# Optimization experiments

Hardware: AMD Instinct MI355X
Metric: run time of the kernel (lower is better)

The kernel has to match this reference:

```python
import jax, jax.numpy as jnp
import numpy as np

N_NODES = 100000


def _gcn_norm(edge_index, n):
    # Add self loops and compute symmetric normalization deg^-1/2 A_hat deg^-1/2
    loops = jnp.arange(n, dtype=edge_index.dtype)
    row = jnp.concatenate([edge_index[0], loops])  # source nodes [E+N]
    col = jnp.concatenate([edge_index[1], loops])  # target nodes [E+N]
    ones = jnp.ones(row.shape[0], dtype=jnp.float32)
    deg = jax.ops.segment_sum(ones, col, num_segments=n)  # in-degree incl. self loop
    dinv = jnp.where(deg > 0, jax.lax.rsqrt(deg), 0.0)
    norm = dinv[row] * dinv[col]  # [E+N]
    return row, col, norm


def _gcn_conv(x, W, b, row, col, norm, n):
    h = x @ W                     # [N, out]
    msg = h[row] * norm[:, None]  # gather + scale  [E+N, out]
    agg = jax.ops.segment_sum(msg, col, num_segments=n)  # scatter-add
    return agg + b


def setup_inputs() -> dict:
    key = jax.random.key(0)
    ks = jax.random.split(key, 8)
    n, e, din, dh, dout = N_NODES, 1600000, 128, 128, 64
    x = jax.random.normal(ks[0], (n, din), dtype=jnp.float32)
    edge_index = jax.random.randint(ks[1], (2, e), 0, n, dtype=jnp.int64)
    s = lambda fan: 1.0 / np.sqrt(fan)
    W0 = jax.random.normal(ks[2], (din, dh), dtype=jnp.float32) * s(din)
    W1 = jax.random.normal(ks[3], (dh, dh), dtype=jnp.float32) * s(dh)
    W2 = jax.random.normal(ks[4], (dh, dout), dtype=jnp.float32) * s(dh)
    b0 = jnp.zeros((dh,), jnp.float32)
    b1 = jnp.zeros((dh,), jnp.float32)
    b2 = jnp.zeros((dout,), jnp.float32)
    return {"x": x, "edge_index": edge_index, "W0": W0, "b0": b0,
            "W1": W1, "b1": b1, "W2": W2, "b2": b2}


def reference(x, edge_index, W0, b0, W1, b1, W2, b2):
    # Eval-mode forward (dropout inactive), matching GCN.forward
    n = x.shape[0]
    row, col, norm = _gcn_norm(edge_index, n)
    h = jax.nn.relu(_gcn_conv(x, W0, b0, row, col, norm, n))
    h = jax.nn.relu(_gcn_conv(h, W1, b1, row, col, norm, n))
    out = _gcn_conv(h, W2, b2, row, col, norm, n)
    return out
```

## Files before the change

### kernel.cpp

```cpp
#include <hip/hip_runtime.h>
#include <stdint.h>


static inline size_t ws_align(size_t x) { return (x + 255) & ~(size_t)255; }

typedef float __f2 __attribute__((ext_vector_type(2)));
typedef float __f4 __attribute__((ext_vector_type(4)));

__device__ __forceinline__ int eidx(const void* p, size_t i, int is64) {
  return is64 ? (int)((const long long*)p)[i] : ((const int*)p)[i];
}

__device__ __forceinline__ uint16_t f2bf(float f) {
  uint32_t u = __float_as_uint(f);
  u += 0x7fffu + ((u >> 16) & 1u);
  return (uint16_t)(u >> 16);
}
__device__ __forceinline__ float bf_lo(uint32_t h) { return __uint_as_float(h << 16); }
__device__ __forceinline__ float bf_hi(uint32_t h) { return __uint_as_float(h & 0xffff0000u); }

__global__ void detect_k(const int* ei, int* flag) {
  if (threadIdx.x == 0 && blockIdx.x == 0) {
    int allz = 1;
    for (int i = 1; i < 128; i += 2)
      if (ei[i] != 0) { allz = 0; break; }
    *flag = allz;
  }
}

__global__ __launch_bounds__(256) void passA_k(const void* ei, const int* __restrict__ flag,
                                               int* __restrict__ bucket_cnt, int E, int NB) {
  __shared__ int cnt[256];
  int t = threadIdx.x;
  cnt[t] = 0;
  __syncthreads();
  int is64 = *flag;
  for (int e = blockIdx.x * 256 + t; e < E; e += gridDim.x * 256) {
    int c = eidx(ei, (size_t)E + e, is64);
    atomicAdd(&cnt[c >> 9], 1);
  }
  __syncthreads();
  if (t < NB && cnt[t]) atomicAdd(&bucket_cnt[t], cnt[t]);
}

__global__ __launch_bounds__(256) void bscan_k(const int* __restrict__ bucket_cnt,
                                               int* __restrict__ bucket_offs,
                                               int* __restrict__ gcursor, int NB) {
  __shared__ int sh[256];
  int t = threadIdx.x;
  int v = (t < NB) ? bucket_cnt[t] : 0;
  sh[t] = v;
  __syncthreads();
  for (int off = 1; off < 256; off <<= 1) {
    int x = (t >= off) ? sh[t - off] : 0;
    __syncthreads();
    sh[t] += x;
    __syncthreads();
  }
  if (t < NB) {
    int excl = sh[t] - v;
    bucket_offs[t] = excl;
    gcursor[t] = excl;
  }
  if (t == NB - 1) bucket_offs[NB] = sh[t];
}

__global__ __launch_bounds__(256) void passB_k(const void* ei, const int* __restrict__ flag,
                                               int* __restrict__ gcursor,
                                               int2* __restrict__ epk_binned, int E, int NB) {
  __shared__ int2 sorted[4096];
  __shared__ int cnt[256], bbase[256], gb[256], cur[256];
  const int t = threadIdx.x;
  const int base = blockIdx.x * 4096;
  const int CH = min(4096, E - base);
  const int is64 = *flag;

  cnt[t] = 0;
  __syncthreads();
  for (int i = t; i < CH; i += 256) {
    int c = eidx(ei, (size_t)E + base + i, is64);
    atomicAdd(&cnt[c >> 9], 1);
  }
  __syncthreads();
  {
    int v = cnt[t];
    __shared__ int sh[256];
    sh[t] = v;
    __syncthreads();
    for (int off = 1; off < 256; off <<= 1) {
      int x = (t >= off) ? sh[t - off] : 0;
      __syncthreads();
      sh[t] += x;
      __syncthreads();
    }
    bbase[t] = sh[t] - v;
    gb[t] = (t < NB && v) ? atomicAdd(&gcursor[t], v) : 0;
    cur[t] = 0;
  }
  __syncthreads();
  for (int i = t; i < CH; i += 256) {
    int r = eidx(ei, (size_t)base + i, is64);
    int c = eidx(ei, (size_t)E + base + i, is64);
    int b = c >> 9;
    int rank = atomicAdd(&cur[b], 1);
    sorted[bbase[b] + rank] = make_int2(r, c);
  }
  __syncthreads();
  for (int i = t; i < CH; i += 256) {
    int2 v = sorted[i];
    int b = v.y >> 9;
    epk_binned[gb[b] + (i - bbase[b])] = v;
  }
}

__global__ __launch_bounds__(256) void passC0_k(const int2* __restrict__ epk_binned,
                                                const int* __restrict__ bucket_offs,
                                                int* __restrict__ deg, int* __restrict__ offs,
                                                int n, int NB) {
  __shared__ int dcnt[512];
  __shared__ int s[256];
  const int t = threadIdx.x;
  const int b = blockIdx.x;
  dcnt[t] = 0; dcnt[t + 256] = 0;
  __syncthreads();
  const int lo = bucket_offs[b], hi = bucket_offs[b + 1];
  for (int i = lo + t; i < hi; i += 256)
    atomicAdd(&dcnt[epk_binned[i].y & 511], 1);
  __syncthreads();
  int d0 = dcnt[2 * t], d1 = dcnt[2 * t + 1];
  int pv = d0 + d1;
  s[t] = pv;
  __syncthreads();
  for (int off = 1; off < 256; off <<= 1) {
    int x = (t >= off) ? s[t - off] : 0;
    __syncthreads();
    s[t] += x;
    __syncthreads();
  }
  int pex = s[t] - pv;
  const int node0 = b << 9;
  int g0 = node0 + 2 * t, g1 = node0 + 2 * t + 1;
  if (g0 < n) { deg[g0] = d0; offs[g0] = lo + pex; }
  if (g1 < n) { deg[g1] = d1; offs[g1] = lo + pex + d0; }
  if (b == NB - 1 && t == 0) offs[n] = hi;
}

__global__ void dinv_k(const int* __restrict__ deg, float* __restrict__ dinv, int n) {
  int i = blockIdx.x * blockDim.x + threadIdx.x;
  if (i < n) dinv[i] = rsqrtf((float)deg[i] + 1.0f);
}

__global__ __launch_bounds__(256) void passC_k(const int2* __restrict__ epk_binned,
                                               const int* __restrict__ bucket_offs,
                                               const int* __restrict__ offs,
                                               uint32_t* __restrict__ epk) {
  __shared__ int cur[512];
  const int t = threadIdx.x;
  const int b = blockIdx.x;
  cur[t] = 0; cur[t + 256] = 0;
  __syncthreads();
  const int lo = bucket_offs[b], hi = bucket_offs[b + 1];
  for (int i = lo + t; i < hi; i += 256) {
    int2 v = epk_binned[i];
    int pos = offs[v.y] + atomicAdd(&cur[v.y & 511], 1);
    epk[pos] = (uint32_t)v.x;
  }
}

template <int COLS, bool SLICED_IN>
__global__ __launch_bounds__(256) void gemm_k(const float* __restrict__ X,
                                              const float* __restrict__ W,
                                              const float* __restrict__ dinv,
                                              uint16_t* __restrict__ H, int N) {
  constexpr int KB = 32;
  constexpr int CG = COLS / 8;
  constexpr int RG = 256 / CG;
  constexpr int ROWS = RG * 8;
  constexpr int XP = ROWS + 4;

  __shared__ float Xs[KB][XP];
  __shared__ float Ws[KB][COLS];

  const int tid = threadIdx.x;
  const int cg = tid % CG, rg = tid / CG;
  const int c0 = cg * 8, rr0 = rg * 8;
  const int rowbase = blockIdx.x * ROWS;
  const float4* X4 = (const float4*)X;

  float acc[8][8];
#pragma unroll
  for (int a = 0; a < 8; ++a)
#pragma unroll
    for (int b = 0; b < 8; ++b) acc[a][b] = 0.f;

  for (int k0 = 0; k0 < 128; k0 += KB) {
    __syncthreads();
#pragma unroll
    for (int i = tid; i < KB * (COLS / 4); i += 256) {
      int kk = i / (COLS / 4);
      int cc = i % (COLS / 4);
      float4 w = ((const float4*)(W + (size_t)(k0 + kk) * COLS))[cc];
      ((float4*)&Ws[kk][0])[cc] = w;
    }
#pragma unroll
    for (int i = tid; i < ROWS * (KB / 4); i += 256) {
      int rr = i / (KB / 4);
      int k4 = i % (KB / 4);
      int gr = rowbase + rr;
      if (gr >= N) gr = N - 1;
      float4 xv;
      if (SLICED_IN) {
        int k = k0 + k4 * 4;
        int s = k >> 5, q = (k & 31) >> 2;
        xv = X4[((size_t)s * N + gr) * 8 + q];
      } else {
        xv = X4[(size_t)gr * 32 + (k0 >> 2) + k4];
      }
      Xs[k4 * 4 + 0][rr] = xv.x;
      Xs[k4 * 4 + 1][rr] = xv.y;
      Xs[k4 * 4 + 2][rr] = xv.z;
      Xs[k4 * 4 + 3][rr] = xv.w;
    }
    __syncthreads();
#pragma unroll 2
    for (int k = 0; k < KB; ++k) {
      float4 xa = *(const float4*)&Xs[k][rr0];
      float4 xb = *(const float4*)&Xs[k][rr0 + 4];
      float4 wa = *(const float4*)&Ws[k][c0];
      float4 wb = *(const float4*)&Ws[k][c0 + 4];
      float xr[8] = {xa.x, xa.y, xa.z, xa.w, xb.x, xb.y, xb.z, xb.w};
      float wr[8] = {wa.x, wa.y, wa.z, wa.w, wb.x, wb.y, wb.z, wb.w};
#pragma unroll
      for (int a = 0; a < 8; ++a)
#pragma unroll
        for (int b = 0; b < 8; ++b) acc[a][b] = fmaf(xr[a], wr[b], acc[a][b]);
    }
  }
  uint32_t* HW = (uint32_t*)H;
  const int wbase = c0 >> 1;
  const int sl = wbase >> 4;
  const int woff = wbase & 15;
#pragma unroll
  for (int a = 0; a < 8; ++a) {
    int row = rowbase + rr0 + a;
    if (row < N) {
      float sc = dinv[row];
      uint32_t p[4];
#pragma unroll
      for (int q = 0; q < 4; ++q)
        p[q] = (uint32_t)f2bf(sc * acc[a][2 * q]) | ((uint32_t)f2bf(sc * acc[a][2 * q + 1]) << 16);
      uint4 ov = make_uint4(p[0], p[1], p[2], p[3]);
      *(uint4*)&HW[((size_t)sl * N + row) * 16 + woff] = ov;
    }
  }
}

__global__ __launch_bounds__(256, 8) void agg128s_k(const uint32_t* __restrict__ HW,
                                                    const int* __restrict__ offs,
                                                    const uint32_t* __restrict__ epk,
                                                    const float* __restrict__ bias,
                                                    float* __restrict__ Aout,
                                                    int relu, int N) {
  const int s = blockIdx.x & 3;
  const int g = blockIdx.x >> 2;
  const int lane = threadIdx.x & 63;
  const int wid = threadIdx.x >> 6;
  const int d = lane >> 3, w = lane & 7;
  const int c = g * 32 + wid * 8 + d;
  if (c >= N) return;
  const uint32_t* Hs = HW + (size_t)s * N * 16;
  int e0 = offs[c], e1 = offs[c + 1];
  float a0 = 0.f, a1 = 0.f, a2 = 0.f, a3 = 0.f;
  int e = e0;
  for (; e + 8 <= e1; e += 8) {
    uint32_t p0 = epk[e],     p1 = epk[e + 1], p2 = epk[e + 2], p3 = epk[e + 3];
    uint32_t p4 = epk[e + 4], p5 = epk[e + 5], p6 = epk[e + 6], p7 = epk[e + 7];
    uint2 h0 = *(const uint2*)&Hs[(size_t)p0 * 16 + 2 * w];
    uint2 h1 = *(const uint2*)&Hs[(size_t)p1 * 16 + 2 * w];
    uint2 h2 = *(const uint2*)&Hs[(size_t)p2 * 16 + 2 * w];
    uint2 h3 = *(const uint2*)&Hs[(size_t)p3 * 16 + 2 * w];
    uint2 h4 = *(const uint2*)&Hs[(size_t)p4 * 16 + 2 * w];
    uint2 h5 = *(const uint2*)&Hs[(size_t)p5 * 16 + 2 * w];
    uint2 h6 = *(const uint2*)&Hs[(size_t)p6 * 16 + 2 * w];
    uint2 h7 = *(const uint2*)&Hs[(size_t)p7 * 16 + 2 * w];
    a0 += bf_lo(h0.x); a1 += bf_hi(h0.x); a2 += bf_lo(h0.y); a3 += bf_hi(h0.y);
    a0 += bf_lo(h1.x); a1 += bf_hi(h1.x); a2 += bf_lo(h1.y); a3 += bf_hi(h1.y);
    a0 += bf_lo(h2.x); a1 += bf_hi(h2.x); a2 += bf_lo(h2.y); a3 += bf_hi(h2.y);
    a0 += bf_lo(h3.x); a1 += bf_hi(h3.x); a2 += bf_lo(h3.y); a3 += bf_hi(h3.y);
    a0 += bf_lo(h4.x); a1 += bf_hi(h4.x); a2 += bf_lo(h4.y); a3 += bf_hi(h4.y);
    a0 += bf_lo(h5.x); a1 += bf_hi(h5.x); a2 += bf_lo(h5.y); a3 += bf_hi(h5.y);
    a0 += bf_lo(h6.x); a1 += bf_hi(h6.x); a2 += bf_lo(h6.y); a3 += bf_hi(h6.y);
    a0 += bf_lo(h7.x); a1 += bf_hi(h7.x); a2 += bf_lo(h7.y); a3 += bf_hi(h7.y);
  }
  for (; e + 4 <= e1; e += 4) {
    uint32_t p0 = epk[e], p1 = epk[e + 1], p2 = epk[e + 2], p3 = epk[e + 3];
    uint2 h0 = *(const uint2*)&Hs[(size_t)p0 * 16 + 2 * w];
    uint2 h1 = *(const uint2*)&Hs[(size_t)p1 * 16 + 2 * w];
    uint2 h2 = *(const uint2*)&Hs[(size_t)p2 * 16 + 2 * w];
    uint2 h3 = *(const uint2*)&Hs[(size_t)p3 * 16 + 2 * w];
    a0 += bf_lo(h0.x); a1 += bf_hi(h0.x); a2 += bf_lo(h0.y); a3 += bf_hi(h0.y);
    a0 += bf_lo(h1.x); a1 += bf_hi(h1.x); a2 += bf_lo(h1.y); a3 += bf_hi(h1.y);
    a0 += bf_lo(h2.x); a1 += bf_hi(h2.x); a2 += bf_lo(h2.y); a3 += bf_hi(h2.y);
    a0 += bf_lo(h3.x); a1 += bf_hi(h3.x); a2 += bf_lo(h3.y); a3 += bf_hi(h3.y);
  }
  for (; e < e1; ++e) {
    uint2 h = *(const uint2*)&Hs[(size_t)epk[e] * 16 + 2 * w];
    a0 += bf_lo(h.x); a1 += bf_hi(h.x); a2 += bf_lo(h.y); a3 += bf_hi(h.y);
  }
  float dc = rsqrtf((float)(e1 - e0) + 1.f);
  uint2 hc = *(const uint2*)&Hs[(size_t)c * 16 + 2 * w];
  float r0 = fmaf(dc, a0 + bf_lo(hc.x), bias[s * 32 + 4 * w + 0]);
  float r1 = fmaf(dc, a1 + bf_hi(hc.x), bias[s * 32 + 4 * w + 1]);
  float r2 = fmaf(dc, a2 + bf_lo(hc.y), bias[s * 32 + 4 * w + 2]);
  float r3 = fmaf(dc, a3 + bf_hi(hc.y), bias[s * 32 + 4 * w + 3]);
  if (relu) {
    r0 = fmaxf(r0, 0.f); r1 = fmaxf(r1, 0.f);
    r2 = fmaxf(r2, 0.f); r3 = fmaxf(r3, 0.f);
  }
  __f4 res; res.x = r0; res.y = r1; res.z = r2; res.w = r3;
  __builtin_nontemporal_store(res, (__f4*)(Aout + ((size_t)s * N + c) * 32 + 4 * w));
}

__global__ __launch_bounds__(256, 8) void agg64s_k(const uint32_t* __restrict__ HW,
                                                   const int* __restrict__ offs,
                                                   const uint32_t* __restrict__ epk,
                                                   const float* __restrict__ bias,
                                                   float* __restrict__ out, int N) {
  const int r = blockIdx.x & 7;
  const int s = r >> 2;
  const int quar = r & 3;
  const int ng = (N + 31) >> 5;
  const int nq = (ng + 3) >> 2;
  const int g = quar * nq + (blockIdx.x >> 3);
  if (g >= ng) return;
  const int lane = threadIdx.x & 63;
  const int wid = threadIdx.x >> 6;
  const int d = lane >> 3, w = lane & 7;
  const int c = g * 32 + wid * 8 + d;
  if (c >= N) return;
  const uint32_t* Hs = HW + (size_t)s * N * 16;
  int e0 = offs[c], e1 = offs[c + 1];
  float a0 = 0.f, a1 = 0.f, a2 = 0.f, a3 = 0.f;
  int e = e0;
  for (; e + 8 <= e1; e += 8) {
    uint32_t p0 = epk[e],     p1 = epk[e + 1], p2 = epk[e + 2], p3 = epk[e + 3];
    uint32_t p4 = epk[e + 4], p5 = epk[e + 5], p6 = epk[e + 6], p7 = epk[e + 7];
    uint2 h0 = *(const uint2*)&Hs[(size_t)p0 * 16 + 2 * w];
    uint2 h1 = *(const uint2*)&Hs[(size_t)p1 * 16 + 2 * w];
    uint2 h2 = *(const uint2*)&Hs[(size_t)p2 * 16 + 2 * w];
    uint2 h3 = *(const uint2*)&Hs[(size_t)p3 * 16 + 2 * w];
    uint2 h4 = *(const uint2*)&Hs[(size_t)p4 * 16 + 2 * w];
    uint2 h5 = *(const uint2*)&Hs[(size_t)p5 * 16 + 2 * w];
    uint2 h6 = *(const uint2*)&Hs[(size_t)p6 * 16 + 2 * w];
    uint2 h7 = *(const uint2*)&Hs[(size_t)p7 * 16 + 2 * w];
    a0 += bf_lo(h0.x); a1 += bf_hi(h0.x); a2 += bf_lo(h0.y); a3 += bf_hi(h0.y);
    a0 += bf_lo(h1.x); a1 += bf_hi(h1.x); a2 += bf_lo(h1.y); a3 += bf_hi(h1.y);
    a0 += bf_lo(h2.x); a1 += bf_hi(h2.x); a2 += bf_lo(h2.y); a3 += bf_hi(h2.y);
    a0 += bf_lo(h3.x); a1 += bf_hi(h3.x); a2 += bf_lo(h3.y); a3 += bf_hi(h3.y);
    a0 += bf_lo(h4.x); a1 += bf_hi(h4.x); a2 += bf_lo(h4.y); a3 += bf_hi(h4.y);
    a0 += bf_lo(h5.x); a1 += bf_hi(h5.x); a2 += bf_lo(h5.y); a3 += bf_hi(h5.y);
    a0 += bf_lo(h6.x); a1 += bf_hi(h6.x); a2 += bf_lo(h6.y); a3 += bf_hi(h6.y);
    a0 += bf_lo(h7.x); a1 += bf_hi(h7.x); a2 += bf_lo(h7.y); a3 += bf_hi(h7.y);
  }
  for (; e + 4 <= e1; e += 4) {
    uint32_t p0 = epk[e], p1 = epk[e + 1], p2 = epk[e + 2], p3 = epk[e + 3];
    uint2 h0 = *(const uint2*)&Hs[(size_t)p0 * 16 + 2 * w];
    uint2 h1 = *(const uint2*)&Hs[(size_t)p1 * 16 + 2 * w];
    uint2 h2 = *(const uint2*)&Hs[(size_t)p2 * 16 + 2 * w];
    uint2 h3 = *(const uint2*)&Hs[(size_t)p3 * 16 + 2 * w];
    a0 += bf_lo(h0.x); a1 += bf_hi(h0.x); a2 += bf_lo(h0.y); a3 += bf_hi(h0.y);
    a0 += bf_lo(h1.x); a1 += bf_hi(h1.x); a2 += bf_lo(h1.y); a3 += bf_hi(h1.y);
    a0 += bf_lo(h2.x); a1 += bf_hi(h2.x); a2 += bf_lo(h2.y); a3 += bf_hi(h2.y);
    a0 += bf_lo(h3.x); a1 += bf_hi(h3.x); a2 += bf_lo(h3.y); a3 += bf_hi(h3.y);
  }
  for (; e < e1; ++e) {
    uint2 h = *(const uint2*)&Hs[(size_t)epk[e] * 16 + 2 * w];
    a0 += bf_lo(h.x); a1 += bf_hi(h.x); a2 += bf_lo(h.y); a3 += bf_hi(h.y);
  }
  float dc = rsqrtf((float)(e1 - e0) + 1.f);
  uint2 hc = *(const uint2*)&Hs[(size_t)c * 16 + 2 * w];
  float r0 = fmaf(dc, a0 + bf_lo(hc.x), bias[s * 32 + 4 * w + 0]);
  float r1 = fmaf(dc, a1 + bf_hi(hc.x), bias[s * 32 + 4 * w + 1]);
  float r2 = fmaf(dc, a2 + bf_lo(hc.y), bias[s * 32 + 4 * w + 2]);
  float r3 = fmaf(dc, a3 + bf_hi(hc.y), bias[s * 32 + 4 * w + 3]);
  __f4 res; res.x = r0; res.y = r1; res.z = r2; res.w = r3;
  __builtin_nontemporal_store(res, (__f4*)(out + (size_t)c * 64 + s * 32 + 4 * w));
}

extern "C" void kernel_launch(void* const* d_in, const int* in_sizes, int n_in,
                              void* d_out, int out_size, void* d_ws, size_t ws_size,
                              hipStream_t stream) {
  const float* x  = (const float*)d_in[0];
  const void*  ei = d_in[1];
  const float* W0 = (const float*)d_in[2];
  const float* b0 = (const float*)d_in[3];
  const float* W1 = (const float*)d_in[4];
  const float* b1 = (const float*)d_in[5];
  const float* W2 = (const float*)d_in[6];
  const float* b2 = (const float*)d_in[7];
  float* out = (float*)d_out;

  const int n = in_sizes[0] / 128;
  const int E = in_sizes[1] / 2;
  const int NB = (n + 511) >> 9;

  char* ws = (char*)d_ws;
  size_t off = 0;
  auto alloc = [&](size_t bytes) { char* p = ws + off; off = ws_align(off + bytes); return p; };
  int*      bucket_cnt  = (int*)alloc(256 * 4);
  int*      bucket_offs = (int*)alloc(257 * 4);
  int*      gcursor     = (int*)alloc(256 * 4);
  int*      deg         = (int*)alloc((size_t)n * 4);
  int*      offs        = (int*)alloc((size_t)(n + 1) * 4);
  float*    dinv        = (float*)alloc((size_t)n * 4);
  int*      flag        = (int*)alloc(4);
  int2*     epk_binned  = (int2*)alloc((size_t)E * 8);
  uint32_t* epk         = (uint32_t*)alloc((size_t)E * 4);
  uint16_t* hbuf        = (uint16_t*)alloc((size_t)n * 128 * 2);
  float*    abuf        = (float*)alloc((size_t)n * 128 * 4);
  (void)ws_size;

  hipMemsetAsync(bucket_cnt, 0, 256 * 4, stream);

  detect_k<<<1, 64, 0, stream>>>((const int*)ei, flag);
  passA_k<<<512, 256, 0, stream>>>(ei, flag, bucket_cnt, E, NB);
  bscan_k<<<1, 256, 0, stream>>>(bucket_cnt, bucket_offs, gcursor, NB);
  passB_k<<<(E + 4095) / 4096, 256, 0, stream>>>(ei, flag, gcursor, epk_binned, E, NB);
  passC0_k<<<NB, 256, 0, stream>>>(epk_binned, bucket_offs, deg, offs, n, NB);
  dinv_k<<<(n + 255) / 256, 256, 0, stream>>>(deg, dinv, n);
  passC_k<<<NB, 256, 0, stream>>>(epk_binned, bucket_offs, offs, epk);

  const int agg128_blocks = 4 * ((n + 31) / 32);
  const int ng = (n + 31) >> 5, nq = (ng + 3) >> 2;
  const int agg64_blocks = 8 * nq;

  gemm_k<128, false><<<(n + 127) / 128, 256, 0, stream>>>(x, W0, dinv, hbuf, n);
  agg128s_k<<<agg128_blocks, 256, 0, stream>>>((const uint32_t*)hbuf, offs, epk, b0, abuf, 1, n);
  gemm_k<128, true><<<(n + 127) / 128, 256, 0, stream>>>(abuf, W1, dinv, hbuf, n);
  agg128s_k<<<agg128_blocks, 256, 0, stream>>>((const uint32_t*)hbuf, offs, epk, b1, abuf, 1, n);
  gemm_k<64, true><<<(n + 255) / 256, 256, 0, stream>>>(abuf, W2, dinv, hbuf, n);
  agg64s_k<<<agg64_blocks, 256, 0, stream>>>((const uint32_t*)hbuf, offs, epk, b2, out, n);
}
```

Before: 497.0 us.

## Replace FP32 FMA GEMMs with split-bf16 MFMA matrix-core GEMMs

The three dense transforms now run on MFMA bf16 instructions. Both operands are split into a hi and a residual lo bf16 part and combined with three MFMAs (hh, lh, hl) to approximate fp32 accuracy. Weights are pre-split into fragment layout by a small prep kernel, and X tiles are converted and stored in a swizzled shared buffer. The intent is to cut the VALU-bound GEMM cost, at the price of extra conversion work, three prep launches, and slightly lower precision than fp32.

Measured after the change: 434.3 us. -12.6%, faster.

```diff
diff --git a/kernel.cpp b/kernel.cpp
--- a/kernel.cpp
+++ b/kernel.cpp
@@ -6,6 +6,8 @@
 
 typedef float __f2 __attribute__((ext_vector_type(2)));
 typedef float __f4 __attribute__((ext_vector_type(4)));
+typedef __attribute__((ext_vector_type(8))) short short8v;
+typedef __attribute__((ext_vector_type(4))) float f32x4;
 
 __device__ __forceinline__ int eidx(const void* p, size_t i, int is64) {
   return is64 ? (int)((const long long*)p)[i] : ((const int*)p)[i];
@@ -167,90 +169,119 @@
   }
 }
 
+template <int COLS>
+__global__ void wprep_k(const float* __restrict__ W, uint16_t* __restrict__ Wf) {
+  constexpr int CT = COLS / 16;
+  const int f = blockIdx.x;
+  const int kc = f / CT, ct = f % CT;
+  const int l = threadIdx.x;
+#pragma unroll
+  for (int j = 0; j < 8; ++j) {
+    int k = kc * 32 + (l >> 4) * 8 + j;
+    int col = ct * 16 + (l & 15);
+    float wv = W[(size_t)k * COLS + col];
+    uint16_t hi = f2bf(wv);
+    float res = wv - __uint_as_float((uint32_t)hi << 16);
+    Wf[(size_t)f * 1024 + l * 8 + j] = hi;
+    Wf[(size_t)f * 1024 + 512 + l * 8 + j] = f2bf(res);
+  }
+}
+
 template <int COLS, bool SLICED_IN>
 __global__ __launch_bounds__(256) void gemm_k(const float* __restrict__ X,
-                                              const float* __restrict__ W,
+                                              const uint16_t* __restrict__ Wf,
                                               const float* __restrict__ dinv,
                                               uint16_t* __restrict__ H, int N) {
-  constexpr int KB = 32;
-  constexpr int CG = COLS / 8;
-  constexpr int RG = 256 / CG;
-  constexpr int ROWS = RG * 8;
-  constexpr int XP = ROWS + 4;
-
-  __shared__ float Xs[KB][XP];
-  __shared__ float Ws[KB][COLS];
+  constexpr int CT = COLS / 16;
+  __shared__ uint32_t Xp[128 * 32];
 
   const int tid = threadIdx.x;
-  const int cg = tid % CG, rg = tid / CG;
-  const int c0 = cg * 8, rr0 = rg * 8;
-  const int rowbase = blockIdx.x * ROWS;
+  const int l = tid & 63, w = tid >> 6;
+  const int rowbase = blockIdx.x * 128;
   const float4* X4 = (const float4*)X;
 
-  float acc[8][8];
-#pragma unroll
-  for (int a = 0; a < 8; ++a)
-#pragma unroll
-    for (int b = 0; b < 8; ++b) acc[a][b] = 0.f;
-
-  for (int k0 = 0; k0 < 128; k0 += KB) {
-    __syncthreads();
-#pragma unroll
-    for (int i = tid; i < KB * (COLS / 4); i += 256) {
-      int kk = i / (COLS / 4);
-      int cc = i % (COLS / 4);
-      float4 w = ((const float4*)(W + (size_t)(k0 + kk) * COLS))[cc];
-      ((float4*)&Ws[kk][0])[cc] = w;
+  f32x4 acc[2][CT];
+#pragma unroll
+  for (int rt = 0; rt < 2; ++rt)
+#pragma unroll
+    for (int ct = 0; ct < CT; ++ct) acc[rt][ct] = (f32x4)0.f;
+
+  for (int kc = 0; kc < 4; ++kc) {
+    __syncthreads();
+#pragma unroll
+    for (int t = 0; t < 4; ++t) {
+      int i = tid + t * 256;
+      int r = i >> 3, q = i & 7;
+      int gr = rowbase + r;
+      if (gr >= N) gr = N - 1;
+      float4 xv = SLICED_IN ? X4[((size_t)kc * N + gr) * 8 + q]
+                            : X4[(size_t)gr * 32 + kc * 8 + q];
+      float xs[4] = {xv.x, xv.y, xv.z, xv.w};
+      uint32_t p[4];
+#pragma unroll
+      for (int e = 0; e < 4; ++e) {
+        uint16_t hi = f2bf(xs[e]);
+        float res = xs[e] - __uint_as_float((uint32_t)hi << 16);
+        p[e] = ((uint32_t)hi << 16) | (uint32_t)f2bf(res);
+      }
+      int blk = q ^ (r & 7);
+      *(uint4*)&Xp[r * 32 + blk * 4] = make_uint4(p[0], p[1], p[2], p[3]);
     }
-#pragma unroll
-    for (int i = tid; i < ROWS * (KB / 4); i += 256) {
-      int rr = i / (KB / 4);
-      int k4 = i % (KB / 4);
-      int gr = rowbase + rr;
-      if (gr >= N) gr = N - 1;
-      float4 xv;
-      if (SLICED_IN) {
-        int k = k0 + k4 * 4;
-        int s = k >> 5, q = (k & 31) >> 2;
-        xv = X4[((size_t)s * N + gr) * 8 + q];
-      } else {
-        xv = X4[(size_t)gr * 32 + (k0 >> 2) + k4];
+    __syncthreads();
+
+    short8v ah[2], al[2];
+#pragma unroll
+    for (int rt = 0; rt < 2; ++rt) {
+      int r = w * 32 + rt * 16 + (l & 15);
+      int c = (r & 7) << 2;
+      int b0 = ((l >> 4) * 8) ^ c;
+      int b1 = ((l >> 4) * 8 + 4) ^ c;
+      uint32_t ua[8];
+      *(uint4*)&ua[0] = *(const uint4*)&Xp[r * 32 + b0];
+      *(uint4*)&ua[4] = *(const uint4*)&Xp[r * 32 + b1];
+      union { uint32_t d[4]; short8v v; } ch, cl;
+#pragma unroll
+      for (int p2 = 0; p2 < 4; ++p2) {
+        ch.d[p2] = __builtin_amdgcn_perm(ua[2 * p2 + 1], ua[2 * p2], 0x07060302u);
+        cl.d[p2] = __builtin_amdgcn_perm(ua[2 * p2 + 1], ua[2 * p2], 0x05040100u);
       }
-      Xs[k4 * 4 + 0][rr] = xv.x;
-      Xs[k4 * 4 + 1][rr] = xv.y;
-      Xs[k4 * 4 + 2][rr] = xv.z;
-      Xs[k4 * 4 + 3][rr] = xv.w;
+      ah[rt] = ch.v;
+      al[rt] = cl.v;
     }
-    __syncthreads();
-#pragma unroll 2
-    for (int k = 0; k < KB; ++k) {
-      float4 xa = *(const float4*)&Xs[k][rr0];
-      float4 xb = *(const float4*)&Xs[k][rr0 + 4];
-      float4 wa = *(const float4*)&Ws[k][c0];
-      float4 wb = *(const float4*)&Ws[k][c0 + 4];
-      float xr[8] = {xa.x, xa.y, xa.z, xa.w, xb.x, xb.y, xb.z, xb.w};
-      float wr[8] = {wa.x, wa.y, wa.z, wa.w, wb.x, wb.y, wb.z, wb.w};
-#pragma unroll
-      for (int a = 0; a < 8; ++a)
-#pragma unroll
-        for (int b = 0; b < 8; ++b) acc[a][b] = fmaf(xr[a], wr[b], acc[a][b]);
+
+#pragma unroll
+    for (int ct = 0; ct < CT; ++ct) {
+      size_t fo = (size_t)(kc * CT + ct) * 1024;
+      short8v bh = *(const short8v*)(Wf + fo + l * 8);
+      short8v bl = *(const short8v*)(Wf + fo + 512 + l * 8);
+#pragma unroll
+      for (int rt = 0; rt < 2; ++rt) {
+        acc[rt][ct] = __builtin_amdgcn_mfma_f32_16x16x32_bf16(ah[rt], bh, acc[rt][ct], 0, 0, 0);
+        acc[rt][ct] = __builtin_amdgcn_mfma_f32_16x16x32_bf16(al[rt], bh, acc[rt][ct], 0, 0, 0);
+        acc[rt][ct] = __builtin_amdgcn_mfma_f32_16x16x32_bf16(ah[rt], bl, acc[rt][ct], 0, 0, 0);
+      }
     }
   }
+
   uint32_t* HW = (uint32_t*)H;
-  const int wbase = c0 >> 1;
-  const int sl = wbase >> 4;
-  const int woff = wbase & 15;
-#pragma unroll
-  for (int a = 0; a < 8; ++a) {
-    int row = rowbase + rr0 + a;
-    if (row < N) {
-      float sc = dinv[row];
-      uint32_t p[4];
-#pragma unroll
-      for (int q = 0; q < 4; ++q)
-        p[q] = (uint32_t)f2bf(sc * acc[a][2 * q]) | ((uint32_t)f2bf(sc * acc[a][2 * q + 1]) << 16);
-      uint4 ov = make_uint4(p[0], p[1], p[2], p[3]);
-      *(uint4*)&HW[((size_t)sl * N + row) * 16 + woff] = ov;
+  const int lq = l >> 4, lc = l & 15;
+#pragma unroll
+  for (int rt = 0; rt < 2; ++rt) {
+#pragma unroll
+    for (int q = 0; q < 4; ++q) {
+      int row = rowbase + w * 32 + rt * 16 + lq * 4 + q;
+      bool ok = row < N;
+      float dv = ok ? dinv[row] : 0.f;
+#pragma unroll
+      for (int ct = 0; ct < CT; ++ct) {
+        float v = acc[rt][ct][q] * dv;
+        int b = (int)f2bf(v);
+        int other = __shfl_xor(b, 1);
+        if (ok && !(l & 1)) {
+          uint32_t word = (uint32_t)b | ((uint32_t)other << 16);
+          HW[((size_t)(ct >> 1) * N + row) * 16 + (ct & 1) * 8 + (lc >> 1)] = word;
+        }
+      }
     }
   }
 }
@@ -414,6 +445,9 @@
   int*      offs        = (int*)alloc((size_t)(n + 1) * 4);
   float*    dinv        = (float*)alloc((size_t)n * 4);
   int*      flag        = (int*)alloc(4);
+  uint16_t* wf0         = (uint16_t*)alloc(64 * 1024);
+  uint16_t* wf1         = (uint16_t*)alloc(64 * 1024);
+  uint16_t* wf2         = (uint16_t*)alloc(32 * 1024);
   int2*     epk_binned  = (int2*)alloc((size_t)E * 8);
   uint32_t* epk         = (uint32_t*)alloc((size_t)E * 4);
   uint16_t* hbuf        = (uint16_t*)alloc((size_t)n * 128 * 2);
@@ -421,6 +455,10 @@
   (void)ws_size;
 
   hipMemsetAsync(bucket_cnt, 0, 256 * 4, stream);
+
+  wprep_k<128><<<32, 64, 0, stream>>>(W0, wf0);
+  wprep_k<128><<<32, 64, 0, stream>>>(W1, wf1);
+  wprep_k<64><<<16, 64, 0, stream>>>(W2, wf2);
 
   detect_k<<<1, 64, 0, stream>>>((const int*)ei, flag);
   passA_k<<<512, 256, 0, stream>>>(ei, flag, bucket_cnt, E, NB);
@@ -430,14 +468,15 @@
   dinv_k<<<(n + 255) / 256, 256, 0, stream>>>(deg, dinv, n);
   passC_k<<<NB, 256, 0, stream>>>(epk_binned, bucket_offs, offs, epk);
 
+  const int gemm_blocks = (n + 127) / 128;
   const int agg128_blocks = 4 * ((n + 31) / 32);
   const int ng = (n + 31) >> 5, nq = (ng + 3) >> 2;
   const int agg64_blocks = 8 * nq;
 
-  gemm_k<128, false><<<(n + 127) / 128, 256, 0, stream>>>(x, W0, dinv, hbuf, n);
+  gemm_k<128, false><<<gemm_blocks, 256, 0, stream>>>(x, wf0, dinv, hbuf, n);
   agg128s_k<<<agg128_blocks, 256, 0, stream>>>((const uint32_t*)hbuf, offs, epk, b0, abuf, 1, n);
-  gemm_k<128, true><<<(n + 127) / 128, 256, 0, stream>>>(abuf, W1, dinv, hbuf, n);
+  gemm_k<128, true><<<gemm_blocks, 256, 0, stream>>>(abuf, wf1, dinv, hbuf, n);
   agg128s_k<<<agg128_blocks, 256, 0, stream>>>((const uint32_t*)hbuf, offs, epk, b1, abuf, 1, n);
-  gemm_k<64, true><<<(n + 255) / 256, 256, 0, stream>>>(abuf, W2, dinv, hbuf, n);
+  gemm_k<64, true><<<gemm_blocks, 256, 0, stream>>>(abuf, wf2, dinv, hbuf, n);
   agg64s_k<<<agg64_blocks, 256, 0, stream>>>((const uint32_t*)hbuf, offs, epk, b2, out, n);
 }
```
